# Kernel tuning notes

Hardware: AMD Instinct MI355X
Metric: run time of the kernel (lower is better)

## Reference

```python
import jax, jax.numpy as jnp
import numpy as np

MAX_ITER = 3  # matches init kwarg max_iter


def setup_inputs() -> dict:
    key = jax.random.key(0)
    k1, k2, k3, k4 = jax.random.split(key, 4)
    B, S = 4, 160
    return {
        "s_edge": jax.random.normal(k1, (B, S, S), dtype=jnp.float32),
        "s_sib": jax.random.normal(k2, (B, S, S, S), dtype=jnp.float32),
        "s_cop": jax.random.normal(k3, (B, S, S, S), dtype=jnp.float32),
        "s_grd": jax.random.normal(k4, (B, S, S, S), dtype=jnp.float32),
        "mask": jnp.ones((B, S, S), dtype=bool),
    }


def reference(s_edge, s_sib, s_cop, s_grd, mask):
    B, S, _ = mask.shape
    idx = jnp.arange(S)
    # Permute to the [head, mod, (sib), batch] layout used by the torch code.
    mask_p = jnp.transpose(mask, (2, 1, 0))              # [h, m, B]
    # 2nd-order mask: both (h,m) and (h,t) arcs valid, and t != h, t != m
    pair_ok = mask_p[:, None, :, :] & mask_p[:, :, None, :]   # [h, m, t, B]
    t_ok = (idx[:, None, None] != idx[None, None, :]) & (
        idx[None, :, None] != idx[None, None, :])             # [h, m, t]
    mask2o = (pair_ok & t_ok[..., None]).astype(s_edge.dtype)  # [h, m, t, B]

    se = jnp.transpose(s_edge, (2, 1, 0))                 # [h, m, B]
    ss = jnp.transpose(s_sib, (2, 1, 3, 0)) * mask2o      # [h, m, t, B]
    sc = jnp.transpose(s_cop, (2, 1, 3, 0)) * mask2o
    sg = jnp.transpose(s_grd, (2, 1, 3, 0)) * mask2o

    q = jnp.zeros((2, S, S, B), dtype=se.dtype)
    for _ in range(MAX_ITER):
        q1 = jax.nn.softmax(q, axis=0)[1]                 # [h, m, B]
        # f[h,m,b] = sum_t q1[h,t,b]*ss + q1[t,m,b]*sc + q1[m,t,b]*sg
        f = (jnp.einsum('htb,hmtb->hmb', q1, ss)
             + jnp.einsum('tmb,hmtb->hmb', q1, sc)
             + jnp.einsum('mtb,hmtb->hmb', q1, sg))
        q = jnp.stack([jnp.zeros_like(f), se + f])        # [2, h, m, B]

    logQ = jax.nn.log_softmax(jnp.transpose(q, (3, 2, 1, 0)), axis=-1)  # [B, m, h... -> B,S,S,2]
    return jnp.exp(logQ)
```

## Files before the change

### kernel.cpp

```cpp
#include <hip/hip_runtime.h>
#include <cmath>

constexpr int S = 160;
constexpr int BATCH = 4;
constexpr int ZSPLIT = 2;
constexpr int ROWS = S / ZSPLIT;
constexpr int KC = S / 4;
constexpr int CHUNKS = ROWS * KC;
constexpr int TPB = 256;
constexpr int FULL_STEPS = CHUNKS / TPB;
constexpr int TAIL = CHUNKS - FULL_STEPS * TPB;

__device__ __forceinline__ float sigmoidf_(float x) {
  return 1.0f / (1.0f + expf(-x));
}

__global__ void prep_wf(const int* __restrict__ mask, unsigned char* __restrict__ wf) {
  int i = blockIdx.x * blockDim.x + threadIdx.x;
  if (i >= BATCH * S * S) return;
  int t = i % S;
  int bh = i / S;
  int h = bh % S;
  int b = bh / S;
  wf[i] = (mask[(b * S + t) * S + h] != 0 && t != h) ? 1 : 0;
}

template <bool FIRST, bool LAST>
__global__ __launch_bounds__(TPB, 5) void mfvi_iter(
    const float* __restrict__ s_edge,
    const float* __restrict__ s_sib,
    const float* __restrict__ s_cop,
    const float* __restrict__ s_grd,
    const int* __restrict__ mask,
    const unsigned char* __restrict__ wf,
    const float* __restrict__ q1_in,
    float* __restrict__ q1_out,
    float* __restrict__ outp) {
  const int m = blockIdx.x;
  const int b = blockIdx.y;
  const int z = blockIdx.z;
  const int tid = threadIdx.x;

  __shared__ __align__(16) float part[CHUNKS];
  __shared__ __align__(16) float colm[S];
  __shared__ __align__(16) float rowm[S];
  __shared__ float sef[ROWS];
  __shared__ float pmf[ROWS];

  const float* G = q1_in + (size_t)b * S * S;
  const size_t bm = (size_t)b * S + m;
  const int h0 = z * ROWS;

  if (tid < S) {
    if (!FIRST) {
      colm[tid] = G[tid * S + m];
      rowm[tid] = G[m * S + tid];
    }
    if (tid < ROWS) {
      sef[tid] = s_edge[bm * S + h0 + tid];
      pmf[tid] = (mask[bm * S + h0 + tid] != 0) ? 1.0f : 0.0f;
    }
  }
  __syncthreads();

  const size_t blk = (bm * S + h0) * (size_t)S;
  const float4* SS = (const float4*)(s_sib + blk);
  const float4* CC = (const float4*)(s_cop + blk);
  const float4* GG = (const float4*)(s_grd + blk);
  const float4* QQ = (const float4*)(G + h0 * S);
  const unsigned* WF = (const unsigned*)(wf + ((size_t)b * S + h0) * S);
  const int msel = m >> 2;
  const unsigned mclr = ~(255u << ((m & 3) * 8));

  auto body = [&](int c) {
    unsigned wu = WF[c];
    float4 s = SS[c];
    float4 cv = CC[c];
    float4 g = GG[c];
    int k = c % KC;
    if (k == msel) wu &= mclr;
    float w0 = (float)(wu & 255u);
    float w1 = (float)((wu >> 8) & 255u);
    float w2 = (float)((wu >> 16) & 255u);
    float w3 = (float)(wu >> 24);
    float p;
    if (FIRST) {
      float t0 = s.x + cv.x + g.x;
      float t1 = s.y + cv.y + g.y;
      float t2 = s.z + cv.z + g.z;
      float t3 = s.w + cv.w + g.w;
      p = fmaf(w0, t0, fmaf(w1, t1, fmaf(w2, t2, w3 * t3)));
    } else {
      float4 q = QQ[c];
      float4 cm = ((const float4*)colm)[k];
      float4 rm = ((const float4*)rowm)[k];
      float t0 = fmaf(q.x, s.x, fmaf(cm.x, cv.x, rm.x * g.x));
      float t1 = fmaf(q.y, s.y, fmaf(cm.y, cv.y, rm.y * g.y));
      float t2 = fmaf(q.z, s.z, fmaf(cm.z, cv.z, rm.z * g.z));
      float t3 = fmaf(q.w, s.w, fmaf(cm.w, cv.w, rm.w * g.w));
      p = fmaf(w0, t0, fmaf(w1, t1, fmaf(w2, t2, w3 * t3)));
    }
    part[c] = p;
  };

  for (int step = 0; step < FULL_STEPS; ++step) body(step * TPB + tid);
  if (tid < TAIL) body(FULL_STEPS * TPB + tid);
  __syncthreads();

  if (tid < ROWS) {
    const float4* pr = (const float4*)part + tid * (KC / 4);
    float4 a = pr[0];
#pragma unroll
    for (int i = 1; i < KC / 4; ++i) {
      float4 v = pr[i];
      a.x += v.x; a.y += v.y; a.z += v.z; a.w += v.w;
    }
    float acc = (a.x + a.y) + (a.z + a.w);
    const int h = h0 + tid;
    const float qv = fmaf(pmf[tid], FIRST ? 0.5f * acc : acc, sef[tid]);
    if (!LAST) {
      q1_out[((size_t)b * S + h) * S + m] = sigmoidf_(qv);
    } else {
      float2 o;
      o.x = sigmoidf_(-qv);
      o.y = sigmoidf_(qv);
      ((float2*)outp)[bm * S + h] = o;
    }
  }
}

extern "C" void kernel_launch(void* const* d_in, const int* in_sizes, int n_in,
                              void* d_out, int out_size, void* d_ws, size_t ws_size,
                              hipStream_t stream) {
  const float* s_edge = (const float*)d_in[0];
  const float* s_sib = (const float*)d_in[1];
  const float* s_cop = (const float*)d_in[2];
  const float* s_grd = (const float*)d_in[3];
  const int* mask = (const int*)d_in[4];
  float* outp = (float*)d_out;

  const int qn = BATCH * S * S;
  float* q1A = (float*)d_ws;
  float* q1B = q1A + qn;
  unsigned char* wf = (unsigned char*)(q1B + qn);

  prep_wf<<<(qn + 255) / 256, 256, 0, stream>>>(mask, wf);

  dim3 grid(S, BATCH, ZSPLIT);
  mfvi_iter<true, false><<<grid, TPB, 0, stream>>>(
      s_edge, s_sib, s_cop, s_grd, mask, wf, q1A, q1B, nullptr);
  mfvi_iter<false, false><<<grid, TPB, 0, stream>>>(
      s_edge, s_sib, s_cop, s_grd, mask, wf, q1B, q1A, nullptr);
  mfvi_iter<false, true><<<grid, TPB, 0, stream>>>(
      s_edge, s_sib, s_cop, s_grd, mask, wf, q1A, nullptr, outp);
}
```

Measured before the change: 262.2 us.

## Reduce rows with 8-lane groups and shuffles instead of shared-memory partials

Each group of 8 lanes now owns one h-row and accumulates its 40 float4 chunks in registers, then combines them with xor shuffles. This removes the shared-memory partial array, the block-wide barrier and the serial per-row reduction done by only 80 threads. Occupancy hint is lowered from 5 to 4 waves, and each lane's loads now stride by 8 chunks within a row, which may change coalescing and the number of loads in flight.

Measured after the change: 263.3 us. No clear change (+0.5%).

```diff
diff --git a/kernel.cpp b/kernel.cpp
--- a/kernel.cpp
+++ b/kernel.cpp
@@ -6,10 +6,11 @@
 constexpr int ZSPLIT = 2;
 constexpr int ROWS = S / ZSPLIT;
 constexpr int KC = S / 4;
-constexpr int CHUNKS = ROWS * KC;
 constexpr int TPB = 256;
-constexpr int FULL_STEPS = CHUNKS / TPB;
-constexpr int TAIL = CHUNKS - FULL_STEPS * TPB;
+constexpr int LPR = 8;
+constexpr int CPL = KC / LPR;
+constexpr int RPP = TPB / LPR;
+constexpr int PASSES = (ROWS + RPP - 1) / RPP;
 
 __device__ __forceinline__ float sigmoidf_(float x) {
   return 1.0f / (1.0f + expf(-x));
@@ -26,7 +27,7 @@
 }
 
 template <bool FIRST, bool LAST>
-__global__ __launch_bounds__(TPB, 5) void mfvi_iter(
+__global__ __launch_bounds__(TPB, 4) void mfvi_iter(
     const float* __restrict__ s_edge,
     const float* __restrict__ s_sib,
     const float* __restrict__ s_cop,
@@ -41,7 +42,6 @@
   const int z = blockIdx.z;
   const int tid = threadIdx.x;
 
-  __shared__ __align__(16) float part[CHUNKS];
   __shared__ __align__(16) float colm[S];
   __shared__ __align__(16) float rowm[S];
   __shared__ float sef[ROWS];
@@ -72,59 +72,60 @@
   const int msel = m >> 2;
   const unsigned mclr = ~(255u << ((m & 3) * 8));
 
-  auto body = [&](int c) {
-    unsigned wu = WF[c];
-    float4 s = SS[c];
-    float4 cv = CC[c];
-    float4 g = GG[c];
-    int k = c % KC;
-    if (k == msel) wu &= mclr;
-    float w0 = (float)(wu & 255u);
-    float w1 = (float)((wu >> 8) & 255u);
-    float w2 = (float)((wu >> 16) & 255u);
-    float w3 = (float)(wu >> 24);
-    float p;
-    if (FIRST) {
-      float t0 = s.x + cv.x + g.x;
-      float t1 = s.y + cv.y + g.y;
-      float t2 = s.z + cv.z + g.z;
-      float t3 = s.w + cv.w + g.w;
-      p = fmaf(w0, t0, fmaf(w1, t1, fmaf(w2, t2, w3 * t3)));
-    } else {
-      float4 q = QQ[c];
-      float4 cm = ((const float4*)colm)[k];
-      float4 rm = ((const float4*)rowm)[k];
-      float t0 = fmaf(q.x, s.x, fmaf(cm.x, cv.x, rm.x * g.x));
-      float t1 = fmaf(q.y, s.y, fmaf(cm.y, cv.y, rm.y * g.y));
-      float t2 = fmaf(q.z, s.z, fmaf(cm.z, cv.z, rm.z * g.z));
-      float t3 = fmaf(q.w, s.w, fmaf(cm.w, cv.w, rm.w * g.w));
-      p = fmaf(w0, t0, fmaf(w1, t1, fmaf(w2, t2, w3 * t3)));
-    }
-    part[c] = p;
-  };
+  const int g = tid >> 3;
+  const int j = tid & 7;
 
-  for (int step = 0; step < FULL_STEPS; ++step) body(step * TPB + tid);
-  if (tid < TAIL) body(FULL_STEPS * TPB + tid);
-  __syncthreads();
-
-  if (tid < ROWS) {
-    const float4* pr = (const float4*)part + tid * (KC / 4);
-    float4 a = pr[0];
 #pragma unroll
-    for (int i = 1; i < KC / 4; ++i) {
-      float4 v = pr[i];
-      a.x += v.x; a.y += v.y; a.z += v.z; a.w += v.w;
-    }
-    float acc = (a.x + a.y) + (a.z + a.w);
-    const int h = h0 + tid;
-    const float qv = fmaf(pmf[tid], FIRST ? 0.5f * acc : acc, sef[tid]);
-    if (!LAST) {
-      q1_out[((size_t)b * S + h) * S + m] = sigmoidf_(qv);
-    } else {
-      float2 o;
-      o.x = sigmoidf_(-qv);
-      o.y = sigmoidf_(qv);
-      ((float2*)outp)[bm * S + h] = o;
+  for (int p = 0; p < PASSES; ++p) {
+    const int r = p * RPP + g;
+    if (r < ROWS) {
+      const int rowbase = r * KC;
+      float acc = 0.0f;
+#pragma unroll
+      for (int i = 0; i < CPL; ++i) {
+        const int k = j + i * LPR;
+        const int c = rowbase + k;
+        unsigned wu = WF[c];
+        float4 s = SS[c];
+        float4 cv = CC[c];
+        float4 gv = GG[c];
+        if (k == msel) wu &= mclr;
+        float w0 = (float)(wu & 255u);
+        float w1 = (float)((wu >> 8) & 255u);
+        float w2 = (float)((wu >> 16) & 255u);
+        float w3 = (float)(wu >> 24);
+        if (FIRST) {
+          float t0 = s.x + cv.x + gv.x;
+          float t1 = s.y + cv.y + gv.y;
+          float t2 = s.z + cv.z + gv.z;
+          float t3 = s.w + cv.w + gv.w;
+          acc = fmaf(w0, t0, fmaf(w1, t1, fmaf(w2, t2, fmaf(w3, t3, acc))));
+        } else {
+          float4 q = QQ[c];
+          float4 cm = ((const float4*)colm)[k];
+          float4 rm = ((const float4*)rowm)[k];
+          float t0 = fmaf(q.x, s.x, fmaf(cm.x, cv.x, rm.x * gv.x));
+          float t1 = fmaf(q.y, s.y, fmaf(cm.y, cv.y, rm.y * gv.y));
+          float t2 = fmaf(q.z, s.z, fmaf(cm.z, cv.z, rm.z * gv.z));
+          float t3 = fmaf(q.w, s.w, fmaf(cm.w, cv.w, rm.w * gv.w));
+          acc = fmaf(w0, t0, fmaf(w1, t1, fmaf(w2, t2, fmaf(w3, t3, acc))));
+        }
+      }
+      acc += __shfl_xor(acc, 1);
+      acc += __shfl_xor(acc, 2);
+      acc += __shfl_xor(acc, 4);
+      if (j == 0) {
+        const int h = h0 + r;
+        const float qv = fmaf(pmf[r], FIRST ? 0.5f * acc : acc, sef[r]);
+        if (!LAST) {
+          q1_out[((size_t)b * S + h) * S + m] = sigmoidf_(qv);
+        } else {
+          float2 o;
+          o.x = sigmoidf_(-qv);
+          o.y = sigmoidf_(qv);
+          ((float2*)outp)[bm * S + h] = o;
+        }
+      }
     }
   }
 }
```
